# Kernel optimization log

Measured on AMD Instinct MI355X. Metric: run time of the kernel, lower is better.

## Reference

```python
import jax, jax.numpy as jnp
import numpy as np

N_NODES = 50000
N_EDGES = 1_600_000
N_QUERY = 100_000
D_FEAT = 128


def setup_inputs() -> dict:
    key = jax.random.key(0)
    k1, k2, k3 = jax.random.split(key, 3)
    x = jax.random.normal(k1, (N_NODES, D_FEAT), dtype=jnp.float32)
    edges = jax.random.randint(k2, (2, N_QUERY), 0, N_NODES, dtype=jnp.int64)
    edge_index = jax.random.randint(k3, (2, N_EDGES), 0, N_NODES, dtype=jnp.int64)
    return {"x": x, "edges": edges, "edge_index": edge_index}


def reference(x, edges, edge_index):
    N = x.shape[0]
    row, col = edge_index[0], edge_index[1]

    # one-hop degree: row-sum of the (binary) adjacency, computed BEFORE normalization
    deg = jax.ops.segment_sum(jnp.ones(row.shape[0], dtype=x.dtype), row, num_segments=N)

    # symmetric normalization D^{-1/2} A D^{-1/2}
    dinv = jnp.where(deg > 0, jax.lax.rsqrt(jnp.maximum(deg, 1e-12)), 0.0)
    val = dinv[row] * dinv[col]  # [E]

    def spmm(feat):  # A_norm @ feat via gather + scatter-add
        return jax.ops.segment_sum(val[:, None] * feat[col], row, num_segments=N)

    one_hop = spmm(x)        # [N, d]
    two_hop = spmm(one_hop)  # [N, d] == (A@A@x); gathering rows equals adj_t[subset] @ one_hop

    u, v = edges[0], edges[1]
    h1u, h1v = one_hop[u], one_hop[v]   # [Q, d]
    h2u, h2v = two_hop[u], two_hop[v]   # [Q, d]
    deg_u, deg_v = deg[u], deg[v]

    count_1_1 = h1u * h1v
    count_1_2 = h1u * h2v
    count_2_1 = h2u * h1v
    count_2_2 = (h2u - deg_u[:, None] * x[u]) * (h2v - deg_v[:, None] * x[v])
    count_self_1_2 = h1u * h2u
    count_self_2_1 = h1v * h2v

    return (count_1_1, count_1_2, count_2_1, count_2_2,
            count_self_1_2, count_self_2_1, deg_u, deg_v)
```

## Files before the change

kernel.cpp:

```cpp
#include <hip/hip_runtime.h>


static constexpr int D = 128;

__global__ __launch_bounds__(256) void k_degree(const int* __restrict__ row,
                                                int* __restrict__ degi, int E) {
    int i = blockIdx.x * blockDim.x + threadIdx.x;
    if (i < E) atomicAdd(&degi[row[i]], 1);
}

__global__ __launch_bounds__(1024) void k_scan(const int* __restrict__ degi,
                                               int* __restrict__ rowptr, int N) {
    __shared__ int buf[1024];
    __shared__ int carry;
    int t = threadIdx.x;
    if (t == 0) { carry = 0; rowptr[0] = 0; }
    __syncthreads();
    for (int base = 0; base < N; base += 1024) {
        int i = base + t;
        int v = (i < N) ? degi[i] : 0;
        buf[t] = v;
        __syncthreads();
        for (int off = 1; off < 1024; off <<= 1) {
            int add = (t >= off) ? buf[t - off] : 0;
            __syncthreads();
            buf[t] += add;
            __syncthreads();
        }
        if (i < N) rowptr[i + 1] = buf[t] + carry;
        __syncthreads();
        if (t == 0) carry += buf[1023];
        __syncthreads();
    }
}

__global__ __launch_bounds__(256) void k_degdinv(const int* __restrict__ degi,
                                                 float* __restrict__ deg,
                                                 float* __restrict__ dinv, int N) {
    int i = blockIdx.x * blockDim.x + threadIdx.x;
    if (i < N) {
        float d = (float)degi[i];
        deg[i] = d;
        dinv[i] = (d > 0.0f) ? (1.0f / sqrtf(d)) : 0.0f;
    }
}

__global__ __launch_bounds__(256) void k_scatter(const int* __restrict__ row,
                                                 const int* __restrict__ col,
                                                 const int* __restrict__ rowptr,
                                                 int* __restrict__ cursor,
                                                 const float* __restrict__ dinv,
                                                 int* __restrict__ csr_col,
                                                 float* __restrict__ csr_val, int E) {
    int e = blockIdx.x * blockDim.x + threadIdx.x;
    if (e < E) {
        int r = row[e];
        int c = col[e];
        int pos = atomicAdd(&cursor[r], 1);
        int idx = rowptr[r] + pos;
        csr_col[idx] = c;
        csr_val[idx] = dinv[r] * dinv[c];
    }
}

__global__ __launch_bounds__(256) void k_spmm_csr(const int* __restrict__ rowptr,
                                                  const int* __restrict__ csr_col,
                                                  const float* __restrict__ csr_val,
                                                  const float* __restrict__ feat,
                                                  float* __restrict__ out, int N) {
    int r = blockIdx.x * 4 + (threadIdx.x >> 6);
    if (r >= N) return;
    int lane = threadIdx.x & 63;
    int beg = rowptr[r];
    int end = rowptr[r + 1];
    float accx = 0.0f, accy = 0.0f;
    for (int j0 = beg; j0 < end; j0 += 64) {
        int navail = end - j0;
        int jj = j0 + lane;
        int cg = (lane < navail) ? csr_col[jj] : 0;
        float wg = (lane < navail) ? csr_val[jj] : 0.0f;
        int m = navail < 64 ? navail : 64;
        for (int k = 0; k < m; ++k) {
            int ck = __shfl(cg, k);
            float wk = __shfl(wg, k);
            float2 xv = ((const float2*)(feat + (size_t)ck * D))[lane];
            accx = fmaf(wk, xv.x, accx);
            accy = fmaf(wk, xv.y, accy);
        }
    }
    float2 o;
    o.x = accx; o.y = accy;
    ((float2*)(out + (size_t)r * D))[lane] = o;
}

__device__ __forceinline__ float4 f4mul(float4 a, float4 b) {
    return make_float4(a.x * b.x, a.y * b.y, a.z * b.z, a.w * b.w);
}
__device__ __forceinline__ float4 f4subs(float4 b, float s, float4 a) {
    return make_float4(b.x - s * a.x, b.y - s * a.y, b.z - s * a.z, b.w - s * a.w);
}

__global__ __launch_bounds__(256) void k_query(const int* __restrict__ U,
                                               const int* __restrict__ V,
                                               const float* __restrict__ x,
                                               const float* __restrict__ h1,
                                               const float* __restrict__ h2,
                                               const float* __restrict__ deg,
                                               float* __restrict__ out, int Q) {
    int t = blockIdx.x * blockDim.x + threadIdx.x;
    int q = t >> 5;
    if (q >= Q) return;
    int lane = t & 31;
    int u = U[q];
    int v = V[q];
    float du = deg[u];
    float dv = deg[v];

    const float4* xf  = (const float4*)x;
    const float4* h1f = (const float4*)h1;
    const float4* h2f = (const float4*)h2;
    size_t ub = (size_t)u * (D / 4) + lane;
    size_t vb = (size_t)v * (D / 4) + lane;

    float4 xu  = xf[ub],  xv  = xf[vb];
    float4 a1u = h1f[ub], a1v = h1f[vb];
    float4 a2u = h2f[ub], a2v = h2f[vb];

    size_t QD4 = (size_t)Q * (D / 4);
    size_t qb  = (size_t)q * (D / 4) + lane;
    float4* of = (float4*)out;

    of[0 * QD4 + qb] = f4mul(a1u, a1v);
    of[1 * QD4 + qb] = f4mul(a1u, a2v);
    of[2 * QD4 + qb] = f4mul(a2u, a1v);
    of[3 * QD4 + qb] = f4mul(f4subs(a2u, du, xu), f4subs(a2v, dv, xv));
    of[4 * QD4 + qb] = f4mul(a1u, a2u);
    of[5 * QD4 + qb] = f4mul(a1v, a2v);

    if (lane == 0) {
        float* tail = out + 6 * (size_t)Q * D;
        tail[q]     = du;
        tail[Q + q] = dv;
    }
}

extern "C" void kernel_launch(void* const* d_in, const int* in_sizes, int n_in,
                              void* d_out, int out_size, void* d_ws, size_t ws_size,
                              hipStream_t stream) {
    const float* x     = (const float*)d_in[0];
    const int*   edges = (const int*)d_in[1];
    const int*   eidx  = (const int*)d_in[2];

    const int N = in_sizes[0] / D;
    const int Q = in_sizes[1] / 2;
    const int E = in_sizes[2] / 2;

    const int* U   = edges;
    const int* V   = edges + Q;
    const int* row = eidx;
    const int* col = eidx + E;

    int Npad = ((N + 1 + 3) / 4) * 4;
    int*   degi    = (int*)d_ws;
    int*   cursor  = degi + N;
    int*   rowptr  = cursor + N;
    float* deg     = (float*)(rowptr + Npad);
    float* dinv    = deg + N;
    int*   csr_col = (int*)(dinv + N);
    float* csr_val = (float*)(csr_col + E);
    float* h1      = csr_val + E;
    float* h2      = h1 + (size_t)N * D;

    hipMemsetAsync(degi, 0, (size_t)2 * N * sizeof(int), stream);

    float* out = (float*)d_out;

    k_degree<<<(E + 255) / 256, 256, 0, stream>>>(row, degi, E);
    k_scan<<<1, 1024, 0, stream>>>(degi, rowptr, N);
    k_degdinv<<<(N + 255) / 256, 256, 0, stream>>>(degi, deg, dinv, N);
    k_scatter<<<(E + 255) / 256, 256, 0, stream>>>(row, col, rowptr, cursor, dinv,
                                                   csr_col, csr_val, E);
    k_spmm_csr<<<(N + 3) / 4, 256, 0, stream>>>(rowptr, csr_col, csr_val, x, h1, N);
    k_spmm_csr<<<(N + 3) / 4, 256, 0, stream>>>(rowptr, csr_col, csr_val, h1, h2, N);
    k_query<<<(Q + 7) / 8, 256, 0, stream>>>(U, V, x, h1, h2, deg, out, Q);
}
```

Measured before the change: 873.6 us.

## Parallelize row-pointer scan, pack CSR col/val, unroll SpMM gathers by four

Replaces the single-block sequential prefix scan over all nodes with a three-pass multi-block scan. The third pass also computes deg/dinv and zeroes the cursor array, which removes one kernel and halves the memset. CSR column and weight are packed into one int2 so each edge needs a single load. The SpMM inner loop is unrolled by four so several feature-row gathers are in flight at once, at the cost of more registers and a tail loop.

```diff
diff --git a/kernel.cpp b/kernel.cpp
--- a/kernel.cpp
+++ b/kernel.cpp
@@ -2,6 +2,7 @@
 
 
 static constexpr int D = 128;
+static constexpr int SCAN_B = 256;
 
 __global__ __launch_bounds__(256) void k_degree(const int* __restrict__ row,
                                                 int* __restrict__ degi, int E) {
@@ -9,36 +10,61 @@
     if (i < E) atomicAdd(&degi[row[i]], 1);
 }
 
-__global__ __launch_bounds__(1024) void k_scan(const int* __restrict__ degi,
-                                               int* __restrict__ rowptr, int N) {
-    __shared__ int buf[1024];
+__global__ __launch_bounds__(SCAN_B) void k_scan1(const int* __restrict__ degi,
+                                                  int* __restrict__ part,
+                                                  int* __restrict__ bsum, int N) {
+    __shared__ int buf[SCAN_B];
+    int t = threadIdx.x;
+    int i = blockIdx.x * SCAN_B + t;
+    int v = (i < N) ? degi[i] : 0;
+    buf[t] = v;
+    __syncthreads();
+    for (int off = 1; off < SCAN_B; off <<= 1) {
+        int a = (t >= off) ? buf[t - off] : 0;
+        __syncthreads();
+        buf[t] += a;
+        __syncthreads();
+    }
+    if (i < N) part[i] = buf[t];
+    if (t == SCAN_B - 1) bsum[blockIdx.x] = buf[t];
+}
+
+__global__ __launch_bounds__(SCAN_B) void k_scan2(int* __restrict__ bsum, int nb) {
+    __shared__ int buf[SCAN_B];
     __shared__ int carry;
     int t = threadIdx.x;
-    if (t == 0) { carry = 0; rowptr[0] = 0; }
+    if (t == 0) carry = 0;
     __syncthreads();
-    for (int base = 0; base < N; base += 1024) {
+    for (int base = 0; base < nb; base += SCAN_B) {
         int i = base + t;
-        int v = (i < N) ? degi[i] : 0;
+        int v = (i < nb) ? bsum[i] : 0;
         buf[t] = v;
         __syncthreads();
-        for (int off = 1; off < 1024; off <<= 1) {
-            int add = (t >= off) ? buf[t - off] : 0;
+        for (int off = 1; off < SCAN_B; off <<= 1) {
+            int a = (t >= off) ? buf[t - off] : 0;
             __syncthreads();
-            buf[t] += add;
+            buf[t] += a;
             __syncthreads();
         }
-        if (i < N) rowptr[i + 1] = buf[t] + carry;
-        __syncthreads();
-        if (t == 0) carry += buf[1023];
-        __syncthreads();
-    }
-}
-
-__global__ __launch_bounds__(256) void k_degdinv(const int* __restrict__ degi,
-                                                 float* __restrict__ deg,
-                                                 float* __restrict__ dinv, int N) {
+        if (i < nb) bsum[i] = buf[t] - v + carry;
+        __syncthreads();
+        if (t == 0) carry += buf[SCAN_B - 1];
+        __syncthreads();
+    }
+}
+
+__global__ __launch_bounds__(256) void k_scan3(const int* __restrict__ part,
+                                               const int* __restrict__ bsum,
+                                               const int* __restrict__ degi,
+                                               int* __restrict__ rowptr,
+                                               int* __restrict__ cursor,
+                                               float* __restrict__ deg,
+                                               float* __restrict__ dinv, int N) {
     int i = blockIdx.x * blockDim.x + threadIdx.x;
     if (i < N) {
+        rowptr[i + 1] = part[i] + bsum[i >> 8];
+        if (i == 0) rowptr[0] = 0;
+        cursor[i] = 0;
         float d = (float)degi[i];
         deg[i] = d;
         dinv[i] = (d > 0.0f) ? (1.0f / sqrtf(d)) : 0.0f;
@@ -50,22 +76,22 @@
                                                  const int* __restrict__ rowptr,
                                                  int* __restrict__ cursor,
                                                  const float* __restrict__ dinv,
-                                                 int* __restrict__ csr_col,
-                                                 float* __restrict__ csr_val, int E) {
+                                                 int2* __restrict__ csr, int E) {
     int e = blockIdx.x * blockDim.x + threadIdx.x;
     if (e < E) {
         int r = row[e];
         int c = col[e];
         int pos = atomicAdd(&cursor[r], 1);
         int idx = rowptr[r] + pos;
-        csr_col[idx] = c;
-        csr_val[idx] = dinv[r] * dinv[c];
+        int2 cw;
+        cw.x = c;
+        cw.y = __float_as_int(dinv[r] * dinv[c]);
+        csr[idx] = cw;
     }
 }
 
 __global__ __launch_bounds__(256) void k_spmm_csr(const int* __restrict__ rowptr,
-                                                  const int* __restrict__ csr_col,
-                                                  const float* __restrict__ csr_val,
+                                                  const int2* __restrict__ csr,
                                                   const float* __restrict__ feat,
                                                   float* __restrict__ out, int N) {
     int r = blockIdx.x * 4 + (threadIdx.x >> 6);
@@ -73,24 +99,42 @@
     int lane = threadIdx.x & 63;
     int beg = rowptr[r];
     int end = rowptr[r + 1];
+    const float2* f2 = (const float2*)feat;
     float accx = 0.0f, accy = 0.0f;
     for (int j0 = beg; j0 < end; j0 += 64) {
-        int navail = end - j0;
-        int jj = j0 + lane;
-        int cg = (lane < navail) ? csr_col[jj] : 0;
-        float wg = (lane < navail) ? csr_val[jj] : 0.0f;
-        int m = navail < 64 ? navail : 64;
-        for (int k = 0; k < m; ++k) {
-            int ck = __shfl(cg, k);
-            float wk = __shfl(wg, k);
-            float2 xv = ((const float2*)(feat + (size_t)ck * D))[lane];
+        int m = end - j0;
+        if (m > 64) m = 64;
+        int2 cw = (lane < m) ? csr[j0 + lane] : make_int2(0, 0);
+        int k = 0;
+        for (; k + 4 <= m; k += 4) {
+            int c0 = __shfl(cw.x, k);
+            int c1 = __shfl(cw.x, k + 1);
+            int c2 = __shfl(cw.x, k + 2);
+            int c3 = __shfl(cw.x, k + 3);
+            float w0 = __int_as_float(__shfl(cw.y, k));
+            float w1 = __int_as_float(__shfl(cw.y, k + 1));
+            float w2 = __int_as_float(__shfl(cw.y, k + 2));
+            float w3 = __int_as_float(__shfl(cw.y, k + 3));
+            float2 x0 = f2[(size_t)c0 * 64 + lane];
+            float2 x1 = f2[(size_t)c1 * 64 + lane];
+            float2 x2 = f2[(size_t)c2 * 64 + lane];
+            float2 x3 = f2[(size_t)c3 * 64 + lane];
+            accx = fmaf(w0, x0.x, accx); accy = fmaf(w0, x0.y, accy);
+            accx = fmaf(w1, x1.x, accx); accy = fmaf(w1, x1.y, accy);
+            accx = fmaf(w2, x2.x, accx); accy = fmaf(w2, x2.y, accy);
+            accx = fmaf(w3, x3.x, accx); accy = fmaf(w3, x3.y, accy);
+        }
+        for (; k < m; ++k) {
+            int ck = __shfl(cw.x, k);
+            float wk = __int_as_float(__shfl(cw.y, k));
+            float2 xv = f2[(size_t)ck * 64 + lane];
             accx = fmaf(wk, xv.x, accx);
             accy = fmaf(wk, xv.y, accy);
         }
     }
     float2 o;
     o.x = accx; o.y = accy;
-    ((float2*)(out + (size_t)r * D))[lane] = o;
+    ((float2*)out)[(size_t)r * 64 + lane] = o;
 }
 
 __device__ __forceinline__ float4 f4mul(float4 a, float4 b) {
@@ -160,27 +204,33 @@
     const int* row = eidx;
     const int* col = eidx + E;
 
+    const int nb = (N + SCAN_B - 1) / SCAN_B;
+
     int Npad = ((N + 1 + 3) / 4) * 4;
-    int*   degi    = (int*)d_ws;
-    int*   cursor  = degi + N;
-    int*   rowptr  = cursor + N;
-    float* deg     = (float*)(rowptr + Npad);
-    float* dinv    = deg + N;
-    int*   csr_col = (int*)(dinv + N);
-    float* csr_val = (float*)(csr_col + E);
-    float* h1      = csr_val + E;
-    float* h2      = h1 + (size_t)N * D;
-
-    hipMemsetAsync(degi, 0, (size_t)2 * N * sizeof(int), stream);
+    int nbpad = ((nb + 3) / 4) * 4;
+    int*   degi   = (int*)d_ws;
+    int*   part   = degi + N;
+    int*   bsum   = part + N;
+    int*   rowptr = bsum + nbpad;
+    int*   cursor = rowptr + Npad;
+    float* deg    = (float*)(cursor + N);
+    float* dinv   = deg + N;
+    int2*  csr    = (int2*)(dinv + N);
+    float* h1     = (float*)(csr + E);
+    float* h2     = h1 + (size_t)N * D;
+
+    hipMemsetAsync(degi, 0, (size_t)N * sizeof(int), stream);
 
     float* out = (float*)d_out;
 
     k_degree<<<(E + 255) / 256, 256, 0, stream>>>(row, degi, E);
-    k_scan<<<1, 1024, 0, stream>>>(degi, rowptr, N);
-    k_degdinv<<<(N + 255) / 256, 256, 0, stream>>>(degi, deg, dinv, N);
+    k_scan1<<<nb, SCAN_B, 0, stream>>>(degi, part, bsum, N);
+    k_scan2<<<1, SCAN_B, 0, stream>>>(bsum, nb);
+    k_scan3<<<(N + 255) / 256, 256, 0, stream>>>(part, bsum, degi, rowptr, cursor,
+                                                 deg, dinv, N);
     k_scatter<<<(E + 255) / 256, 256, 0, stream>>>(row, col, rowptr, cursor, dinv,
-                                                   csr_col, csr_val, E);
-    k_spmm_csr<<<(N + 3) / 4, 256, 0, stream>>>(rowptr, csr_col, csr_val, x, h1, N);
-    k_spmm_csr<<<(N + 3) / 4, 256, 0, stream>>>(rowptr, csr_col, csr_val, h1, h2, N);
+                                                   csr, E);
+    k_spmm_csr<<<(N + 3) / 4, 256, 0, stream>>>(rowptr, csr, x, h1, N);
+    k_spmm_csr<<<(N + 3) / 4, 256, 0, stream>>>(rowptr, csr, h1, h2, N);
     k_query<<<(Q + 7) / 8, 256, 0, stream>>>(U, V, x, h1, h2, deg, out, Q);
 }
```

Result: faster. 742.7 us (-15.0%).
